# Kernel optimization log

Measured on AMD Instinct MI355X. Metric: run time of the kernel, lower is better.

## Reference

```python
import jax, jax.numpy as jnp
import numpy as np

N_NODES = 50000
N_EDGES = 800000
DIM = 64
N_LAYERS = 3
LN_EPS = 1e-5


def setup_inputs() -> dict:
    key = jax.random.key(0)
    k_x, k_e, k_w = jax.random.split(key, 3)
    x = jax.random.normal(k_x, (N_NODES, DIM), dtype=jnp.float32)
    edge_index = jax.random.randint(k_e, (2, N_EDGES), 0, N_NODES, dtype=jnp.int32)
    # GCNConv params: weight [in, out] (glorot-ish), bias zeros
    Ws = jax.random.normal(k_w, (N_LAYERS, DIM, DIM), dtype=jnp.float32) / np.sqrt(DIM)
    bs = jnp.zeros((N_LAYERS, DIM), dtype=jnp.float32)
    # LayerNorm params
    gammas = jnp.ones((N_LAYERS, DIM), dtype=jnp.float32)
    betas = jnp.zeros((N_LAYERS, DIM), dtype=jnp.float32)
    return {"x": x, "edge_index": edge_index, "Ws": Ws, "bs": bs,
            "gammas": gammas, "betas": betas}


def reference(x, edge_index, Ws, bs, gammas, betas):
    n = x.shape[0]
    # GCN normalization with self-loops (PyG gcn_norm, add_self_loops=True)
    loops = jnp.arange(n, dtype=edge_index.dtype)
    src = jnp.concatenate([edge_index[0], loops])  # [E + N]
    dst = jnp.concatenate([edge_index[1], loops])
    deg = jax.ops.segment_sum(jnp.ones(src.shape[0], x.dtype), dst, num_segments=n)
    dinv = jax.lax.rsqrt(deg)  # deg >= 1 because of self-loops
    norm = (dinv[src] * dinv[dst])[:, None]  # [E+N, 1]

    for i in range(Ws.shape[0]):  # fixed, small layer count
        h = x @ Ws[i]  # [N, D] dense transform
        # sparse-dense aggregation: gather -> scale -> scatter-add
        h = jax.ops.segment_sum(h[src] * norm, dst, num_segments=n) + bs[i]
        # LayerNorm over features
        mu = jnp.mean(h, axis=-1, keepdims=True)
        var = jnp.var(h, axis=-1, keepdims=True)
        h = (h - mu) * jax.lax.rsqrt(var + LN_EPS) * gammas[i] + betas[i]
        # dropout is identity in eval mode; then relu
        x = jax.nn.relu(h)
    return x
```

## Files before the change

### kernel.cpp

```cpp
#include <hip/hip_runtime.h>

#define DIM 64
#define LN_EPS 1e-5f
#define XS_STRIDE 68
#define RPB 16


__global__ void k_zero(int* __restrict__ deg, int* __restrict__ counter, int n) {
    int i = blockIdx.x * blockDim.x + threadIdx.x;
    if (i < n) deg[i] = 0;
    if (i == 0) { counter[0] = 0; counter[1] = 0; }
}

__global__ void k_count(const int* __restrict__ dst, int* __restrict__ deg,
                        int* __restrict__ rank, int e_cnt) {
    int e = blockIdx.x * blockDim.x + threadIdx.x;
    if (e < e_cnt) rank[e] = atomicAdd(&deg[dst[e]], 1);
}

__global__ void k_reserve(const int* __restrict__ deg, int* __restrict__ rowstart,
                          float* __restrict__ dinv,
                          int* __restrict__ counter, int n) {
    int i = blockIdx.x * blockDim.x + threadIdx.x;
    if (i >= n) return;
    int d = deg[i];
    int s = atomicAdd(counter, d);
    rowstart[i] = s;
    dinv[i] = rsqrtf((float)(d + 1));
}

__global__ void k_fill(const int* __restrict__ src, const int* __restrict__ dst,
                       const float* __restrict__ dinv,
                       const int* __restrict__ rowstart,
                       const int* __restrict__ rank,
                       int2* __restrict__ csr, int e_cnt) {
    int e = blockIdx.x * blockDim.x + threadIdx.x;
    if (e >= e_cnt) return;
    int s = src[e], d = dst[e];
    int pos = rowstart[d] + rank[e];
    float w = dinv[s] * dinv[d];
    csr[pos] = make_int2(s, __float_as_int(w));
}

__global__ __launch_bounds__(256) void k_layer(const int* __restrict__ rowstart,
                                               const int* __restrict__ deg,
                                               const float* __restrict__ dinv,
                                               const int2* __restrict__ csr,
                                               const float* __restrict__ xin,
                                               const float* __restrict__ W,
                                               const float* __restrict__ b,
                                               const float* __restrict__ gamma,
                                               const float* __restrict__ beta,
                                               float* __restrict__ out, int n) {
    __shared__ float ws[DIM * DIM];
    __shared__ float xs[RPB * XS_STRIDE];
    int t = threadIdx.x;
    int base = blockIdx.x * RPB;

    {
        const float4* W4 = (const float4*)W;
        float4* ws4 = (float4*)ws;
#pragma unroll
        for (int i = 0; i < 4; i++) ws4[t + 256 * i] = W4[t + 256 * i];
    }

    int wave = t >> 6, lane = t & 63;
    int rs = lane >> 4;
    int fq = lane & 15;
    int lrow = wave * 4 + rs;
    int row = base + lrow;
    const float4* xin4 = (const float4*)xin;

    float4 acc = make_float4(0.f, 0.f, 0.f, 0.f);
    if (row < n) {
        int s0 = rowstart[row];
        int cnt = deg[row];
        int i = 0;
        for (; i + 4 <= cnt; i += 4) {
            int2 e0 = csr[s0 + i + 0];
            int2 e1 = csr[s0 + i + 1];
            int2 e2 = csr[s0 + i + 2];
            int2 e3 = csr[s0 + i + 3];
            float4 h0 = xin4[(size_t)e0.x * 16 + fq];
            float4 h1 = xin4[(size_t)e1.x * 16 + fq];
            float4 h2 = xin4[(size_t)e2.x * 16 + fq];
            float4 h3 = xin4[(size_t)e3.x * 16 + fq];
            float w0 = __int_as_float(e0.y);
            float w1 = __int_as_float(e1.y);
            float w2 = __int_as_float(e2.y);
            float w3 = __int_as_float(e3.y);
            acc.x = fmaf(w0, h0.x, acc.x);
            acc.y = fmaf(w0, h0.y, acc.y);
            acc.z = fmaf(w0, h0.z, acc.z);
            acc.w = fmaf(w0, h0.w, acc.w);
            acc.x = fmaf(w1, h1.x, acc.x);
            acc.y = fmaf(w1, h1.y, acc.y);
            acc.z = fmaf(w1, h1.z, acc.z);
            acc.w = fmaf(w1, h1.w, acc.w);
            acc.x = fmaf(w2, h2.x, acc.x);
            acc.y = fmaf(w2, h2.y, acc.y);
            acc.z = fmaf(w2, h2.z, acc.z);
            acc.w = fmaf(w2, h2.w, acc.w);
            acc.x = fmaf(w3, h3.x, acc.x);
            acc.y = fmaf(w3, h3.y, acc.y);
            acc.z = fmaf(w3, h3.z, acc.z);
            acc.w = fmaf(w3, h3.w, acc.w);
        }
        for (; i < cnt; i++) {
            int2 e0 = csr[s0 + i];
            float4 h0 = xin4[(size_t)e0.x * 16 + fq];
            float w0 = __int_as_float(e0.y);
            acc.x = fmaf(w0, h0.x, acc.x);
            acc.y = fmaf(w0, h0.y, acc.y);
            acc.z = fmaf(w0, h0.z, acc.z);
            acc.w = fmaf(w0, h0.w, acc.w);
        }
        float di = dinv[row];
        float w = di * di;
        float4 xv = xin4[(size_t)row * 16 + fq];
        acc.x = fmaf(w, xv.x, acc.x);
        acc.y = fmaf(w, xv.y, acc.y);
        acc.z = fmaf(w, xv.z, acc.z);
        acc.w = fmaf(w, xv.w, acc.w);
    }
    *(float4*)(xs + lrow * XS_STRIDE + fq * 4) = acc;
    __syncthreads();

    float4 a2 = make_float4(0.f, 0.f, 0.f, 0.f);
    for (int kc = 0; kc < 16; kc++) {
        float4 xv = *(const float4*)(xs + lrow * XS_STRIDE + kc * 4);
        float4 w0 = *(const float4*)(ws + (4 * kc + 0) * DIM + fq * 4);
        float4 w1 = *(const float4*)(ws + (4 * kc + 1) * DIM + fq * 4);
        float4 w2 = *(const float4*)(ws + (4 * kc + 2) * DIM + fq * 4);
        float4 w3 = *(const float4*)(ws + (4 * kc + 3) * DIM + fq * 4);
        a2.x = fmaf(xv.x, w0.x, a2.x);
        a2.y = fmaf(xv.x, w0.y, a2.y);
        a2.z = fmaf(xv.x, w0.z, a2.z);
        a2.w = fmaf(xv.x, w0.w, a2.w);
        a2.x = fmaf(xv.y, w1.x, a2.x);
        a2.y = fmaf(xv.y, w1.y, a2.y);
        a2.z = fmaf(xv.y, w1.z, a2.z);
        a2.w = fmaf(xv.y, w1.w, a2.w);
        a2.x = fmaf(xv.z, w2.x, a2.x);
        a2.y = fmaf(xv.z, w2.y, a2.y);
        a2.z = fmaf(xv.z, w2.z, a2.z);
        a2.w = fmaf(xv.z, w2.w, a2.w);
        a2.x = fmaf(xv.w, w3.x, a2.x);
        a2.y = fmaf(xv.w, w3.y, a2.y);
        a2.z = fmaf(xv.w, w3.z, a2.z);
        a2.w = fmaf(xv.w, w3.w, a2.w);
    }

    float4 b4 = *(const float4*)(b + fq * 4);
    float4 g4 = *(const float4*)(gamma + fq * 4);
    float4 be4 = *(const float4*)(beta + fq * 4);

    float4 v = make_float4(a2.x + b4.x, a2.y + b4.y, a2.z + b4.z, a2.w + b4.w);
    float s = v.x + v.y + v.z + v.w;
    s += __shfl_xor(s, 1, 64);
    s += __shfl_xor(s, 2, 64);
    s += __shfl_xor(s, 4, 64);
    s += __shfl_xor(s, 8, 64);
    float mu = s * (1.0f / 64.0f);
    float4 d = make_float4(v.x - mu, v.y - mu, v.z - mu, v.w - mu);
    float q = d.x * d.x + d.y * d.y + d.z * d.z + d.w * d.w;
    q += __shfl_xor(q, 1, 64);
    q += __shfl_xor(q, 2, 64);
    q += __shfl_xor(q, 4, 64);
    q += __shfl_xor(q, 8, 64);
    float rstd = rsqrtf(q * (1.0f / 64.0f) + LN_EPS);
    float4 y = make_float4(fmaxf(fmaf(d.x * rstd, g4.x, be4.x), 0.f),
                           fmaxf(fmaf(d.y * rstd, g4.y, be4.y), 0.f),
                           fmaxf(fmaf(d.z * rstd, g4.z, be4.z), 0.f),
                           fmaxf(fmaf(d.w * rstd, g4.w, be4.w), 0.f));
    if (row < n)
        *(float4*)(out + (size_t)row * DIM + fq * 4) = y;
}


extern "C" void kernel_launch(void* const* d_in, const int* in_sizes, int n_in,
                              void* d_out, int out_size, void* d_ws, size_t ws_size,
                              hipStream_t stream) {
    const float* x      = (const float*)d_in[0];
    const int*   ei     = (const int*)  d_in[1];
    const float* Ws     = (const float*)d_in[2];
    const float* bs     = (const float*)d_in[3];
    const float* gammas = (const float*)d_in[4];
    const float* betas  = (const float*)d_in[5];
    float* out = (float*)d_out;

    int n = in_sizes[0] / DIM;
    int E = in_sizes[1] / 2;
    int n_layers = in_sizes[2] / (DIM * DIM);

    const int* srcp = ei;
    const int* dstp = ei + E;

    int* deg      = (int*)d_ws;
    int* rowstart = deg + n;
    float* dinv   = (float*)(rowstart + n);
    int* counter  = (int*)(dinv + n);
    int* rank     = counter + 2;
    int2* csr     = (int2*)(rank + E);
    float* bufA   = (float*)(csr + E);

    int nb_n = (n + 255) / 256;
    int nb_e = (E + 255) / 256;

    k_zero   <<<nb_n, 256, 0, stream>>>(deg, counter, n);
    k_count  <<<nb_e, 256, 0, stream>>>(dstp, deg, rank, E);
    k_reserve<<<nb_n, 256, 0, stream>>>(deg, rowstart, dinv, counter, n);
    k_fill   <<<nb_e, 256, 0, stream>>>(srcp, dstp, dinv, rowstart, rank, csr, E);

    int nb_tile = (n + RPB - 1) / RPB;
    const float* src_buf = x;
    for (int i = 0; i < n_layers; i++) {
        float* dst = (((n_layers - 1 - i) & 1) == 0) ? out : bufA;
        k_layer<<<nb_tile, 256, 0, stream>>>(rowstart, deg, dinv, csr, src_buf,
                                             Ws + (size_t)i * DIM * DIM,
                                             bs + (size_t)i * DIM,
                                             gammas + (size_t)i * DIM,
                                             betas + (size_t)i * DIM, dst, n);
        src_buf = dst;
    }
}
```

Measured before the change: 252.5 us.

## Assign one wave per row and split edges across lane groups

Each wave now handles a single node instead of four. The four 16-lane subgroups split that node's edge list, and later the K dimension of the 64x64 transform, with partial sums combined by cross-lane shuffles. The goal is to balance the irregular per-row degree work and give more parallel gather loads per row. The cost is four times as many blocks, each still loading the full 16KB weight matrix into shared memory, plus extra shuffle reductions and lanes that sit idle during the LayerNorm and store.

After: 280.0 us. 10.9% more time.

```diff
diff --git a/kernel.cpp b/kernel.cpp
--- a/kernel.cpp
+++ b/kernel.cpp
@@ -3,7 +3,7 @@
 #define DIM 64
 #define LN_EPS 1e-5f
 #define XS_STRIDE 68
-#define RPB 16
+#define RPB 4
 
 
 __global__ void k_zero(int* __restrict__ deg, int* __restrict__ counter, int n) {
@@ -65,10 +65,9 @@
     }
 
     int wave = t >> 6, lane = t & 63;
-    int rs = lane >> 4;
+    int es = lane >> 4;
     int fq = lane & 15;
-    int lrow = wave * 4 + rs;
-    int row = base + lrow;
+    int row = base + wave;
     const float4* xin4 = (const float4*)xin;
 
     float4 acc = make_float4(0.f, 0.f, 0.f, 0.f);
@@ -76,11 +75,11 @@
         int s0 = rowstart[row];
         int cnt = deg[row];
         int i = 0;
-        for (; i + 4 <= cnt; i += 4) {
-            int2 e0 = csr[s0 + i + 0];
-            int2 e1 = csr[s0 + i + 1];
-            int2 e2 = csr[s0 + i + 2];
-            int2 e3 = csr[s0 + i + 3];
+        for (; i + 16 <= cnt; i += 16) {
+            int2 e0 = csr[s0 + i + es];
+            int2 e1 = csr[s0 + i + 4 + es];
+            int2 e2 = csr[s0 + i + 8 + es];
+            int2 e3 = csr[s0 + i + 12 + es];
             float4 h0 = xin4[(size_t)e0.x * 16 + fq];
             float4 h1 = xin4[(size_t)e1.x * 16 + fq];
             float4 h2 = xin4[(size_t)e2.x * 16 + fq];
@@ -106,29 +105,46 @@
             acc.z = fmaf(w3, h3.z, acc.z);
             acc.w = fmaf(w3, h3.w, acc.w);
         }
-        for (; i < cnt; i++) {
-            int2 e0 = csr[s0 + i];
-            float4 h0 = xin4[(size_t)e0.x * 16 + fq];
-            float w0 = __int_as_float(e0.y);
-            acc.x = fmaf(w0, h0.x, acc.x);
-            acc.y = fmaf(w0, h0.y, acc.y);
-            acc.z = fmaf(w0, h0.z, acc.z);
-            acc.w = fmaf(w0, h0.w, acc.w);
+#pragma unroll
+        for (int u = 0; u < 4; u++) {
+            int idx = i + 4 * u + es;
+            if (idx < cnt) {
+                int2 e0 = csr[s0 + idx];
+                float4 h0 = xin4[(size_t)e0.x * 16 + fq];
+                float w0 = __int_as_float(e0.y);
+                acc.x = fmaf(w0, h0.x, acc.x);
+                acc.y = fmaf(w0, h0.y, acc.y);
+                acc.z = fmaf(w0, h0.z, acc.z);
+                acc.w = fmaf(w0, h0.w, acc.w);
+            }
         }
-        float di = dinv[row];
-        float w = di * di;
-        float4 xv = xin4[(size_t)row * 16 + fq];
-        acc.x = fmaf(w, xv.x, acc.x);
-        acc.y = fmaf(w, xv.y, acc.y);
-        acc.z = fmaf(w, xv.z, acc.z);
-        acc.w = fmaf(w, xv.w, acc.w);
-    }
-    *(float4*)(xs + lrow * XS_STRIDE + fq * 4) = acc;
+        if (es == 0) {
+            float di = dinv[row];
+            float w = di * di;
+            float4 xv = xin4[(size_t)row * 16 + fq];
+            acc.x = fmaf(w, xv.x, acc.x);
+            acc.y = fmaf(w, xv.y, acc.y);
+            acc.z = fmaf(w, xv.z, acc.z);
+            acc.w = fmaf(w, xv.w, acc.w);
+        }
+    }
+    acc.x += __shfl_xor(acc.x, 16, 64);
+    acc.y += __shfl_xor(acc.y, 16, 64);
+    acc.z += __shfl_xor(acc.z, 16, 64);
+    acc.w += __shfl_xor(acc.w, 16, 64);
+    acc.x += __shfl_xor(acc.x, 32, 64);
+    acc.y += __shfl_xor(acc.y, 32, 64);
+    acc.z += __shfl_xor(acc.z, 32, 64);
+    acc.w += __shfl_xor(acc.w, 32, 64);
+    if (es == 0)
+        *(float4*)(xs + wave * XS_STRIDE + fq * 4) = acc;
     __syncthreads();
 
     float4 a2 = make_float4(0.f, 0.f, 0.f, 0.f);
-    for (int kc = 0; kc < 16; kc++) {
-        float4 xv = *(const float4*)(xs + lrow * XS_STRIDE + kc * 4);
+#pragma unroll
+    for (int u = 0; u < 4; u++) {
+        int kc = es * 4 + u;
+        float4 xv = *(const float4*)(xs + wave * XS_STRIDE + kc * 4);
         float4 w0 = *(const float4*)(ws + (4 * kc + 0) * DIM + fq * 4);
         float4 w1 = *(const float4*)(ws + (4 * kc + 1) * DIM + fq * 4);
         float4 w2 = *(const float4*)(ws + (4 * kc + 2) * DIM + fq * 4);
@@ -150,6 +166,14 @@
         a2.z = fmaf(xv.w, w3.z, a2.z);
         a2.w = fmaf(xv.w, w3.w, a2.w);
     }
+    a2.x += __shfl_xor(a2.x, 16, 64);
+    a2.y += __shfl_xor(a2.y, 16, 64);
+    a2.z += __shfl_xor(a2.z, 16, 64);
+    a2.w += __shfl_xor(a2.w, 16, 64);
+    a2.x += __shfl_xor(a2.x, 32, 64);
+    a2.y += __shfl_xor(a2.y, 32, 64);
+    a2.z += __shfl_xor(a2.z, 32, 64);
+    a2.w += __shfl_xor(a2.w, 32, 64);
 
     float4 b4 = *(const float4*)(b + fq * 4);
     float4 g4 = *(const float4*)(gamma + fq * 4);
@@ -173,8 +197,9 @@
                            fmaxf(fmaf(d.y * rstd, g4.y, be4.y), 0.f),
                            fmaxf(fmaf(d.z * rstd, g4.z, be4.z), 0.f),
                            fmaxf(fmaf(d.w * rstd, g4.w, be4.w), 0.f));
-    if (row < n)
-        *(float4*)(out + (size_t)row * DIM + fq * 4) = y;
+    int row2 = base + wave;
+    if (row2 < n && es == 0)
+        *(float4*)(out + (size_t)row2 * DIM + fq * 4) = y;
 }
 
 
```
